# Kernel optimization log

Measured on AMD Instinct MI355X. Metric: run time of the kernel, lower is better.

## Reference

```python
import jax, jax.numpy as jnp
import numpy as np

MARGIN = 0.3
BIG = 9999999.0


def setup_inputs() -> dict:
    key = jax.random.key(0)
    k1, k2, k3 = jax.random.split(key, 3)
    N, D, D2, NUM_IDS = 8192, 1024, 512, 512
    emb = jax.random.normal(k1, (N, D), dtype=jnp.float32)
    clot_feats_s = jax.random.normal(k2, (N, D2), dtype=jnp.float32)
    label = jax.random.randint(k3, (N,), 0, NUM_IDS, dtype=jnp.int64)
    return {"emb": emb, "label": label, "clot_feats_s": clot_feats_s}


def _margin_ranking_loss(x1, x2, y, margin):
    # torch MarginRankingLoss: mean(max(0, -y*(x1-x2)+margin))
    return jnp.mean(jnp.maximum(0.0, -y * (x1 - x2) + margin))


def reference(emb, label, clot_feats_s):
    N = emb.shape[0]
    # euclidean_dist(emb, emb): [N,N]
    sq = jnp.sum(emb * emb, axis=1)
    dist = sq[:, None] + sq[None, :] - 2.0 * (emb @ emb.T)
    dist = jnp.sqrt(jnp.clip(dist, 1e-12, None))
    # cosine similarity of clot_feats_s with itself: [N,N]
    nrm = jnp.sqrt(jnp.sum(clot_feats_s * clot_feats_s, axis=1))
    cos = (clot_feats_s @ clot_feats_s.T) / (nrm[:, None] * nrm[None, :])
    # same-identity mask
    sim = (label[:, None] == label[None, :]).astype(dist.dtype)
    # batch-hard: top-2 positives (largest masked distance), hardest negative (smallest)
    pos_vals, pos_idx = jax.lax.top_k(dist - BIG * (1.0 - sim), 2)
    dist_ap1, dist_ap2 = pos_vals[:, 0], pos_vals[:, 1]
    neg_mat = dist + BIG * sim
    hard_n_idx = jnp.argmin(neg_mat, axis=1)
    dist_an = jnp.min(neg_mat, axis=1)
    rows = jnp.arange(N)
    # per-row gathers into cosine-sim matrix (detached in original)
    alpha1 = jax.lax.stop_gradient(cos[rows, pos_idx[:, 0]])
    alpha2 = jax.lax.stop_gradient(cos[rows, pos_idx[:, 1]])
    # (alphan gathered in original but unused in the loss)
    y11 = jnp.where(alpha1 < alpha2, -1.0, 1.0)
    y11_m = jnp.where(alpha1 == alpha2, 0.0, 1.0)
    loss11 = _margin_ranking_loss(
        dist_ap2 * y11_m,
        dist_ap1 * y11_m + MARGIN * (alpha1 - alpha2 - y11),
        y11, MARGIN)
    dist_ap1_m = dist_ap1 + MARGIN * (alpha1 - 1.0)
    loss13 = _margin_ranking_loss(dist_an, dist_ap1_m, 1.0, MARGIN)
    loss = 0.1 * loss11 + loss13
    prec = jnp.mean((dist_an > dist_ap1_m).astype(jnp.float32))
    return loss, prec
```

## Files before the change

kernel.cpp:

```cpp
#include <hip/hip_runtime.h>
#include <stdint.h>

#define NR 8192
#define DE 1024
#define DC 512
#define BIGF 9999999.0f
#define MARG 0.3f
#define NEGI -3.0e38f
#define POSI 3.0e38f

typedef __attribute__((ext_vector_type(8))) short bf16x8;
typedef __attribute__((ext_vector_type(4))) float f32x4;

typedef __attribute__((address_space(3))) unsigned int lds_u32;
typedef const __attribute__((address_space(1))) unsigned int glb_u32;

static __device__ __forceinline__ void ld_g2l16(const void* g, void* l) {
    __builtin_amdgcn_global_load_lds((glb_u32*)g, (lds_u32*)l, 16, 0, 0);
}

static __device__ __forceinline__ unsigned short f2bf(float x) {
    unsigned u = __float_as_uint(x);
    unsigned r = u + 0x7FFFu + ((u >> 16) & 1u);
    return (unsigned short)(r >> 16);
}

static __device__ __forceinline__ float b2f(short u) {
    return __uint_as_float(((unsigned)(unsigned short)u) << 16);
}

__global__ __launch_bounds__(256) void k_prep_emb(const float* __restrict__ emb,
                                                  const int* __restrict__ label,
                                                  short* __restrict__ embb,
                                                  float* __restrict__ sq,
                                                  int* __restrict__ cnt) {
    int row = blockIdx.x, tid = threadIdx.x;
    float4 v = ((const float4*)(emb + (size_t)row * DE))[tid];
    float s = v.x * v.x + v.y * v.y + v.z * v.z + v.w * v.w;
    ushort4 b;
    b.x = f2bf(v.x); b.y = f2bf(v.y); b.z = f2bf(v.z); b.w = f2bf(v.w);
    *(ushort4*)&embb[(size_t)row * DE + tid * 4] = b;
    for (int m = 1; m < 64; m <<= 1) s += __shfl_xor(s, m);
    __shared__ float red[4];
    if ((tid & 63) == 0) red[tid >> 6] = s;
    __syncthreads();
    if (tid == 0) {
        sq[row] = red[0] + red[1] + red[2] + red[3];
        atomicAdd(&cnt[label[row]], 1);
    }
}

__global__ __launch_bounds__(512) void k_scan(const int* __restrict__ cnt,
                                              int* __restrict__ clsOff) {
    __shared__ int s[512];
    int t = threadIdx.x;
    s[t] = cnt[t];
    __syncthreads();
    for (int d = 1; d < 512; d <<= 1) {
        int v = (t >= d) ? s[t - d] : 0;
        __syncthreads();
        s[t] += v;
        __syncthreads();
    }
    clsOff[t] = s[t] - cnt[t];
}

__global__ __launch_bounds__(256) void k_fill(const int* __restrict__ label,
                                              const int* __restrict__ clsOff,
                                              int* __restrict__ fill,
                                              int* __restrict__ list) {
    int i = blockIdx.x * 256 + threadIdx.x;
    int l = label[i];
    int p = atomicAdd(&fill[l], 1);
    list[clsOff[l] + p] = i;
}

__global__ __launch_bounds__(256, 3) void k_main(const short* __restrict__ embb,
                                                 const float* __restrict__ sq,
                                                 const int* __restrict__ label,
                                                 unsigned* __restrict__ mnA) {
    const int L = (blockIdx.x & 7) * 68 + (blockIdx.x >> 3);
    int bx = (int)((sqrtf((float)(1 + 2 * L)) - 1.0f) * 0.5f);
    while (2 * (bx + 1) * (bx + 1) + 2 * (bx + 1) <= L) ++bx;
    while (2 * bx * bx + 2 * bx > L) --bx;
    const int pnl = L - (2 * bx * bx + 2 * bx);
    const int d = pnl - bx * 4;
    const int jt0 = d > 0 ? d : 0;

    __shared__ __align__(16) short As[128 * 32];
    __shared__ __align__(16) short Bs[128 * 32];

    const int tid = threadIdx.x;
    const int lane = tid & 63;
    const int w = tid >> 6;
    const int q = lane >> 4, l15 = lane & 15;
    const int i0 = pnl * 128;

    const int srow = tid >> 2;
    const int g = (tid & 3) ^ ((tid >> 3) & 3);
    const short* gA = embb + (size_t)(i0 + srow) * DE + g * 8;
    const short* gB = embb + (size_t)(bx * 512 + jt0 * 128 + srow) * DE + g * 8;

    const int pxor = q ^ ((l15 >> 1) & 3);

    float rmn[8], sqi[8];
    int lia[8];
#pragma unroll
    for (int pp = 0; pp < 8; ++pp) {
        rmn[pp] = POSI;
        int rowg = i0 + w * 32 + (pp >> 2) * 16 + q * 4 + (pp & 3);
        sqi[pp] = sq[rowg]; lia[pp] = label[rowg];
    }

    auto stage = [&](int koff, const short* gBb) {
        ld_g2l16(gA + koff, &As[(size_t)tid * 8]);
        ld_g2l16(gA + (size_t)64 * DE + koff, &As[(size_t)(tid + 256) * 8]);
        ld_g2l16(gBb + koff, &Bs[(size_t)tid * 8]);
        ld_g2l16(gBb + (size_t)64 * DE + koff, &Bs[(size_t)(tid + 256) * 8]);
    };

    stage(0, gB);

    for (int jt = jt0; jt < 4; ++jt) {
        const int j0 = bx * 512 + jt * 128;
        f32x4 acc[2][8];
#pragma unroll
        for (int mi = 0; mi < 2; ++mi)
#pragma unroll
            for (int ni = 0; ni < 8; ++ni) acc[mi][ni] = (f32x4){0.f, 0.f, 0.f, 0.f};

        for (int ks = 0; ks < 32; ++ks) {
            __syncthreads();
            bf16x8 af[2], bfr[8];
#pragma unroll
            for (int mi = 0; mi < 2; ++mi)
                af[mi] = *(const bf16x8*)&As[(w * 32 + mi * 16 + l15) * 32 + pxor * 8];
#pragma unroll
            for (int ni = 0; ni < 8; ++ni)
                bfr[ni] = *(const bf16x8*)&Bs[(ni * 16 + l15) * 32 + pxor * 8];
#pragma unroll
            for (int mi = 0; mi < 2; ++mi)
#pragma unroll
                for (int ni = 0; ni < 8; ++ni)
                    acc[mi][ni] = __builtin_amdgcn_mfma_f32_16x16x32_bf16(af[mi], bfr[ni], acc[mi][ni], 0, 0, 0);
            __syncthreads();
            if (ks < 31) {
                stage((ks + 1) * 32, gB);
            } else if (jt < 3) {
                gB += (size_t)128 * DE;
                stage(0, gB);
            }
        }

#pragma unroll
        for (int ni = 0; ni < 8; ++ni) {
            const int cg = j0 + ni * 16 + l15;
            const float sqjv = sq[cg];
            const int lbjv = label[cg];
            float cmn = POSI;
#pragma unroll
            for (int pp = 0; pp < 8; ++pp) {
                float d2 = fmaf(-2.0f, acc[pp >> 2][ni][pp & 3], sqi[pp] + sqjv);
                d2 = fmaxf(d2, 1e-12f);
                float dn = (lia[pp] == lbjv) ? POSI : d2;
                rmn[pp] = fminf(rmn[pp], dn);
                cmn = fminf(cmn, dn);
            }
            cmn = fminf(cmn, __shfl_xor(cmn, 16));
            cmn = fminf(cmn, __shfl_xor(cmn, 32));
            if (q == 0) atomicMin(&mnA[cg], __float_as_uint(cmn));
        }
    }

#pragma unroll
    for (int pp = 0; pp < 8; ++pp) {
        float m0 = rmn[pp];
        for (int s = 1; s <= 8; s <<= 1) m0 = fminf(m0, __shfl_xor(m0, s));
        if (l15 == 0) {
            int rowg = i0 + w * 32 + (pp >> 2) * 16 + q * 4 + (pp & 3);
            atomicMin(&mnA[rowg], __float_as_uint(m0));
        }
    }
}

__global__ __launch_bounds__(256) void k_pos(const short* __restrict__ embb,
                                             const float* __restrict__ sq,
                                             const float* __restrict__ clot,
                                             const int* __restrict__ label,
                                             const int* __restrict__ cnt,
                                             const int* __restrict__ clsOff,
                                             const int* __restrict__ clsList,
                                             const unsigned* __restrict__ mnA,
                                             float* __restrict__ ap1, float* __restrict__ ap2,
                                             float* __restrict__ an,
                                             float* __restrict__ alpha1, float* __restrict__ alpha2) {
    int wid = threadIdx.x >> 6, lane = threadIdx.x & 63;
    int row = blockIdx.x * 4 + wid;
    int lb = label[row];
    int cc = cnt[lb], off = clsOff[lb];
    float sqiv = sq[row];

    const bf16x8* rp = (const bf16x8*)(embb + (size_t)row * DE + lane * 16);
    bf16x8 ra = rp[0], rb = rp[1];
    float rf[16];
#pragma unroll
    for (int t = 0; t < 8; ++t) { rf[t] = b2f(ra[t]); rf[8 + t] = b2f(rb[t]); }

    float v1 = NEGI, v2 = NEGI;
    int i1 = 0, i2 = 0;
    for (int m = 0; m < cc; ++m) {
        int j = clsList[off + m];
        float d2;
        if (j == row) {
            d2 = 1e-12f;
        } else {
            const bf16x8* jp = (const bf16x8*)(embb + (size_t)j * DE + lane * 16);
            bf16x8 ja = jp[0], jb = jp[1];
            float s = 0.f;
#pragma unroll
            for (int t = 0; t < 8; ++t) s = fmaf(rf[t], b2f(ja[t]), s);
#pragma unroll
            for (int t = 0; t < 8; ++t) s = fmaf(rf[8 + t], b2f(jb[t]), s);
            for (int mm = 1; mm < 64; mm <<= 1) s += __shfl_xor(s, mm);
            d2 = fmaxf(fmaf(-2.0f, s, sqiv + sq[j]), 1e-12f);
        }
        bool t1 = (d2 > v1) || (d2 == v1 && j < i1);
        bool t2 = (d2 > v2) || (d2 == v2 && j < i2);
        v2 = t1 ? v1 : (t2 ? d2 : v2);
        i2 = t1 ? i1 : (t2 ? j : i2);
        v1 = t1 ? d2 : v1;
        i1 = t1 ? j : i1;
    }

    float a1 = sqrtf(v1);
    int j1 = i1;
    float a2v; int j2;
    if (cc >= 2) {
        a2v = sqrtf(v2);
        j2 = i2;
    } else {
        float kv = NEGI; int ki = 0;
        for (int c = lane; c < NR; c += 64) {
            if (label[c] == lb) continue;
            float s = 0.f;
            const short* crow = embb + (size_t)c * DE;
            const short* rrow = embb + (size_t)row * DE;
            for (int t = 0; t < DE; ++t) s = fmaf(b2f(rrow[t]), b2f(crow[t]), s);
            float d2c = fmaxf(fmaf(-2.0f, s, sqiv + sq[c]), 1e-12f);
            bool tk = (d2c > kv) || (d2c == kv && c < ki);
            kv = tk ? d2c : kv; ki = tk ? c : ki;
        }
        for (int mm = 1; mm < 64; mm <<= 1) {
            float ov = __shfl_xor(kv, mm); int oi = __shfl_xor(ki, mm);
            bool tk = (ov > kv) || (ov == kv && oi < ki);
            kv = tk ? ov : kv; ki = tk ? oi : ki;
        }
        a2v = sqrtf(kv) - BIGF;
        j2 = ki;
    }

    const float4* c4 = (const float4*)clot;
    float s1 = 0.f, s2 = 0.f, n0 = 0.f, n1 = 0.f, n2 = 0.f;
    for (int t = lane; t < DC / 4; t += 64) {
        float4 a = c4[(size_t)row * (DC / 4) + t];
        float4 b1 = c4[(size_t)j1 * (DC / 4) + t];
        float4 b2 = c4[(size_t)j2 * (DC / 4) + t];
        s1 += a.x * b1.x + a.y * b1.y + a.z * b1.z + a.w * b1.w;
        s2 += a.x * b2.x + a.y * b2.y + a.z * b2.z + a.w * b2.w;
        n0 += a.x * a.x + a.y * a.y + a.z * a.z + a.w * a.w;
        n1 += b1.x * b1.x + b1.y * b1.y + b1.z * b1.z + b1.w * b1.w;
        n2 += b2.x * b2.x + b2.y * b2.y + b2.z * b2.z + b2.w * b2.w;
    }
    for (int mm = 1; mm < 64; mm <<= 1) {
        s1 += __shfl_xor(s1, mm); s2 += __shfl_xor(s2, mm);
        n0 += __shfl_xor(n0, mm); n1 += __shfl_xor(n1, mm); n2 += __shfl_xor(n2, mm);
    }
    if (lane == 0) {
        ap1[row] = a1; ap2[row] = a2v;
        an[row] = sqrtf(__uint_as_float(mnA[row]));
        alpha1[row] = s1 / (sqrtf(n0) * sqrtf(n1));
        alpha2[row] = s2 / (sqrtf(n0) * sqrtf(n2));
    }
}

__global__ __launch_bounds__(256) void k_final(const float* __restrict__ ap1, const float* __restrict__ ap2,
                                               const float* __restrict__ an,
                                               const float* __restrict__ alpha1, const float* __restrict__ alpha2,
                                               float* __restrict__ out) {
    int tid = threadIdx.x;
    float sl11 = 0.f, sl13 = 0.f, sp = 0.f;
    for (int row = tid; row < NR; row += 256) {
        float a1 = alpha1[row], a2 = alpha2[row];
        float dap1 = ap1[row], dap2 = ap2[row], dan = an[row];
        float y = (a1 < a2) ? -1.f : 1.f;
        float ym = (a1 == a2) ? 0.f : 1.f;
        float x1 = dap2 * ym;
        float x2 = dap1 * ym + MARG * (a1 - a2 - y);
        sl11 += fmaxf(0.f, -y * (x1 - x2) + MARG);
        float ap1m = dap1 + MARG * (a1 - 1.f);
        sl13 += fmaxf(0.f, -(dan - ap1m) + MARG);
        sp += (dan > ap1m) ? 1.f : 0.f;
    }
    for (int m = 1; m < 64; m <<= 1) {
        sl11 += __shfl_xor(sl11, m);
        sl13 += __shfl_xor(sl13, m);
        sp += __shfl_xor(sp, m);
    }
    __shared__ float r11[4], r13[4], rp[4];
    if ((tid & 63) == 0) { r11[tid >> 6] = sl11; r13[tid >> 6] = sl13; rp[tid >> 6] = sp; }
    __syncthreads();
    if (tid == 0) {
        float t11 = r11[0] + r11[1] + r11[2] + r11[3];
        float t13 = r13[0] + r13[1] + r13[2] + r13[3];
        float tp = rp[0] + rp[1] + rp[2] + rp[3];
        out[0] = 0.1f * (t11 / (float)NR) + t13 / (float)NR;
        out[1] = tp / (float)NR;
    }
}

extern "C" void kernel_launch(void* const* d_in, const int* in_sizes, int n_in,
                              void* d_out, int out_size, void* d_ws, size_t ws_size,
                              hipStream_t stream) {
    const float* emb = (const float*)d_in[0];
    const int* label = (const int*)d_in[1];
    const float* clot = (const float*)d_in[2];
    float* out = (float*)d_out;

    char* ws = (char*)d_ws;
    size_t off = 0;
    auto alloc = [&](size_t bytes) -> char* {
        char* p = ws + off;
        off = (off + bytes + 255) & ~(size_t)255;
        return p;
    };
    short*    embb = (short*)alloc((size_t)NR * DE * 2);
    float*    sq   = (float*)alloc(NR * 4);
    int*      cnt  = (int*)alloc(512 * 4);
    int*      cOff = (int*)alloc(512 * 4);
    int*      fill = (int*)alloc(512 * 4);
    int*      list = (int*)alloc(NR * 4);
    unsigned* mnA  = (unsigned*)alloc((size_t)NR * 4);
    float*    ap1  = (float*)alloc(NR * 4);
    float*    ap2  = (float*)alloc(NR * 4);
    float*    an   = (float*)alloc(NR * 4);
    float*    al1  = (float*)alloc(NR * 4);
    float*    al2  = (float*)alloc(NR * 4);

    hipMemsetAsync(cnt, 0, 512 * 4, stream);
    hipMemsetAsync(fill, 0, 512 * 4, stream);
    hipMemsetAsync(mnA, 0xFF, (size_t)NR * 4, stream);

    k_prep_emb<<<dim3(NR), dim3(256), 0, stream>>>(emb, label, embb, sq, cnt);
    k_scan<<<dim3(1), dim3(512), 0, stream>>>(cnt, cOff);
    k_fill<<<dim3(NR / 256), dim3(256), 0, stream>>>(label, cOff, fill, list);
    k_main<<<dim3(544), dim3(256), 0, stream>>>(embb, sq, label, mnA);
    k_pos<<<dim3(NR / 4), dim3(256), 0, stream>>>(embb, sq, clot, label, cnt, cOff, list,
                                                  mnA, ap1, ap2, an, al1, al2);
    k_final<<<dim3(1), dim3(256), 0, stream>>>(ap1, ap2, an, al1, al2, out);
}
```

Baseline: 256.9 us.

## Use square 128x128 triangular tiles in main GEMM and per-class positive kernel

The main distance kernel stops having each block sweep a 128x512 strip and gives each block one 128x128 upper-triangular tile. Warps are laid out 2x2 (64x64 each) instead of 4x1, and the launch grows from 544 to 2080 blocks. The positive-mining kernel now runs one block per identity class and stages up to 48 class member embeddings in LDS, so all rows of the class reuse them instead of each row re-reading members from global memory. The trade-off is more blocks with shorter K loops in the GEMM, about 96KB of LDS per block (limiting occupancy), and load imbalance across classes of different size.

New measurement: 381.2 us. 1.48x slower.

```diff
diff --git a/kernel.cpp b/kernel.cpp
--- a/kernel.cpp
+++ b/kernel.cpp
@@ -8,6 +8,7 @@
 #define MARG 0.3f
 #define NEGI -3.0e38f
 #define POSI 3.0e38f
+#define CAPR 48
 
 typedef __attribute__((ext_vector_type(8))) short bf16x8;
 typedef __attribute__((ext_vector_type(4))) float f32x4;
@@ -79,13 +80,14 @@
                                                  const float* __restrict__ sq,
                                                  const int* __restrict__ label,
                                                  unsigned* __restrict__ mnA) {
-    const int L = (blockIdx.x & 7) * 68 + (blockIdx.x >> 3);
-    int bx = (int)((sqrtf((float)(1 + 2 * L)) - 1.0f) * 0.5f);
-    while (2 * (bx + 1) * (bx + 1) + 2 * (bx + 1) <= L) ++bx;
-    while (2 * bx * bx + 2 * bx > L) --bx;
-    const int pnl = L - (2 * bx * bx + 2 * bx);
-    const int d = pnl - bx * 4;
-    const int jt0 = d > 0 ? d : 0;
+    const int b = blockIdx.x;
+    int r = (int)((129.0f - sqrtf(16641.0f - 8.0f * (float)b)) * 0.5f);
+    if (r < 0) r = 0;
+    if (r > 63) r = 63;
+    while (r > 0 && 64 * r - (r * (r - 1)) / 2 > b) --r;
+    while (64 * (r + 1) - ((r + 1) * r) / 2 <= b) ++r;
+    const int c = r + (b - (64 * r - (r * (r - 1)) / 2));
+    const int i0 = r * 128, j0 = c * 128;
 
     __shared__ __align__(16) short As[128 * 32];
     __shared__ __align__(16) short Bs[128 * 32];
@@ -93,93 +95,91 @@
     const int tid = threadIdx.x;
     const int lane = tid & 63;
     const int w = tid >> 6;
+    const int wr = w >> 1, wc = w & 1;
     const int q = lane >> 4, l15 = lane & 15;
-    const int i0 = pnl * 128;
 
     const int srow = tid >> 2;
     const int g = (tid & 3) ^ ((tid >> 3) & 3);
     const short* gA = embb + (size_t)(i0 + srow) * DE + g * 8;
-    const short* gB = embb + (size_t)(bx * 512 + jt0 * 128 + srow) * DE + g * 8;
+    const short* gB = embb + (size_t)(j0 + srow) * DE + g * 8;
 
     const int pxor = q ^ ((l15 >> 1) & 3);
 
-    float rmn[8], sqi[8];
-    int lia[8];
-#pragma unroll
-    for (int pp = 0; pp < 8; ++pp) {
-        rmn[pp] = POSI;
-        int rowg = i0 + w * 32 + (pp >> 2) * 16 + q * 4 + (pp & 3);
-        sqi[pp] = sq[rowg]; lia[pp] = label[rowg];
-    }
-
-    auto stage = [&](int koff, const short* gBb) {
+    auto stage = [&](int koff) {
         ld_g2l16(gA + koff, &As[(size_t)tid * 8]);
         ld_g2l16(gA + (size_t)64 * DE + koff, &As[(size_t)(tid + 256) * 8]);
-        ld_g2l16(gBb + koff, &Bs[(size_t)tid * 8]);
-        ld_g2l16(gBb + (size_t)64 * DE + koff, &Bs[(size_t)(tid + 256) * 8]);
+        ld_g2l16(gB + koff, &Bs[(size_t)tid * 8]);
+        ld_g2l16(gB + (size_t)64 * DE + koff, &Bs[(size_t)(tid + 256) * 8]);
     };
 
-    stage(0, gB);
-
-    for (int jt = jt0; jt < 4; ++jt) {
-        const int j0 = bx * 512 + jt * 128;
-        f32x4 acc[2][8];
-#pragma unroll
-        for (int mi = 0; mi < 2; ++mi)
-#pragma unroll
-            for (int ni = 0; ni < 8; ++ni) acc[mi][ni] = (f32x4){0.f, 0.f, 0.f, 0.f};
-
-        for (int ks = 0; ks < 32; ++ks) {
-            __syncthreads();
-            bf16x8 af[2], bfr[8];
-#pragma unroll
-            for (int mi = 0; mi < 2; ++mi)
-                af[mi] = *(const bf16x8*)&As[(w * 32 + mi * 16 + l15) * 32 + pxor * 8];
-#pragma unroll
-            for (int ni = 0; ni < 8; ++ni)
-                bfr[ni] = *(const bf16x8*)&Bs[(ni * 16 + l15) * 32 + pxor * 8];
-#pragma unroll
-            for (int mi = 0; mi < 2; ++mi)
-#pragma unroll
-                for (int ni = 0; ni < 8; ++ni)
-                    acc[mi][ni] = __builtin_amdgcn_mfma_f32_16x16x32_bf16(af[mi], bfr[ni], acc[mi][ni], 0, 0, 0);
-            __syncthreads();
-            if (ks < 31) {
-                stage((ks + 1) * 32, gB);
-            } else if (jt < 3) {
-                gB += (size_t)128 * DE;
-                stage(0, gB);
+    stage(0);
+
+    f32x4 acc[4][4];
+#pragma unroll
+    for (int mi = 0; mi < 4; ++mi)
+#pragma unroll
+        for (int ni = 0; ni < 4; ++ni) acc[mi][ni] = (f32x4){0.f, 0.f, 0.f, 0.f};
+
+    for (int ks = 0; ks < 32; ++ks) {
+        __syncthreads();
+        bf16x8 af[4], bfr[4];
+#pragma unroll
+        for (int mi = 0; mi < 4; ++mi)
+            af[mi] = *(const bf16x8*)&As[(wr * 64 + mi * 16 + l15) * 32 + pxor * 8];
+#pragma unroll
+        for (int ni = 0; ni < 4; ++ni)
+            bfr[ni] = *(const bf16x8*)&Bs[(wc * 64 + ni * 16 + l15) * 32 + pxor * 8];
+#pragma unroll
+        for (int mi = 0; mi < 4; ++mi)
+#pragma unroll
+            for (int ni = 0; ni < 4; ++ni)
+                acc[mi][ni] = __builtin_amdgcn_mfma_f32_16x16x32_bf16(af[mi], bfr[ni], acc[mi][ni], 0, 0, 0);
+        __syncthreads();
+        if (ks < 31) stage((ks + 1) * 32);
+    }
+
+    const int rb = i0 + wr * 64, cb = j0 + wc * 64;
+    float sqj[4]; int lbj[4]; float cmn[4];
+#pragma unroll
+    for (int ni = 0; ni < 4; ++ni) {
+        int cg = cb + ni * 16 + l15;
+        sqj[ni] = sq[cg]; lbj[ni] = label[cg]; cmn[ni] = POSI;
+    }
+#pragma unroll
+    for (int mi = 0; mi < 4; ++mi) {
+        float rm[4] = {POSI, POSI, POSI, POSI};
+        float sqi[4]; int lbi[4];
+#pragma unroll
+        for (int rr = 0; rr < 4; ++rr) {
+            int rg = rb + mi * 16 + q * 4 + rr;
+            sqi[rr] = sq[rg]; lbi[rr] = label[rg];
+        }
+#pragma unroll
+        for (int ni = 0; ni < 4; ++ni)
+#pragma unroll
+            for (int rr = 0; rr < 4; ++rr) {
+                float d2 = fmaf(-2.0f, acc[mi][ni][rr], sqi[rr] + sqj[ni]);
+                d2 = fmaxf(d2, 1e-12f);
+                float dn = (lbi[rr] == lbj[ni]) ? POSI : d2;
+                rm[rr] = fminf(rm[rr], dn);
+                cmn[ni] = fminf(cmn[ni], dn);
             }
-        }
-
-#pragma unroll
-        for (int ni = 0; ni < 8; ++ni) {
-            const int cg = j0 + ni * 16 + l15;
-            const float sqjv = sq[cg];
-            const int lbjv = label[cg];
-            float cmn = POSI;
-#pragma unroll
-            for (int pp = 0; pp < 8; ++pp) {
-                float d2 = fmaf(-2.0f, acc[pp >> 2][ni][pp & 3], sqi[pp] + sqjv);
-                d2 = fmaxf(d2, 1e-12f);
-                float dn = (lia[pp] == lbjv) ? POSI : d2;
-                rmn[pp] = fminf(rmn[pp], dn);
-                cmn = fminf(cmn, dn);
-            }
-            cmn = fminf(cmn, __shfl_xor(cmn, 16));
-            cmn = fminf(cmn, __shfl_xor(cmn, 32));
-            if (q == 0) atomicMin(&mnA[cg], __float_as_uint(cmn));
-        }
-    }
-
-#pragma unroll
-    for (int pp = 0; pp < 8; ++pp) {
-        float m0 = rmn[pp];
-        for (int s = 1; s <= 8; s <<= 1) m0 = fminf(m0, __shfl_xor(m0, s));
-        if (l15 == 0) {
-            int rowg = i0 + w * 32 + (pp >> 2) * 16 + q * 4 + (pp & 3);
-            atomicMin(&mnA[rowg], __float_as_uint(m0));
-        }
+#pragma unroll
+        for (int rr = 0; rr < 4; ++rr) {
+            float v = rm[rr];
+            v = fminf(v, __shfl_xor(v, 1));
+            v = fminf(v, __shfl_xor(v, 2));
+            v = fminf(v, __shfl_xor(v, 4));
+            v = fminf(v, __shfl_xor(v, 8));
+            if (l15 == 0) atomicMin(&mnA[rb + mi * 16 + q * 4 + rr], __float_as_uint(v));
+        }
+    }
+#pragma unroll
+    for (int ni = 0; ni < 4; ++ni) {
+        float v = cmn[ni];
+        v = fminf(v, __shfl_xor(v, 16));
+        v = fminf(v, __shfl_xor(v, 32));
+        if (q == 0) atomicMin(&mnA[cb + ni * 16 + l15], __float_as_uint(v));
     }
 }
 
@@ -194,92 +194,116 @@
                                              float* __restrict__ ap1, float* __restrict__ ap2,
                                              float* __restrict__ an,
                                              float* __restrict__ alpha1, float* __restrict__ alpha2) {
-    int wid = threadIdx.x >> 6, lane = threadIdx.x & 63;
-    int row = blockIdx.x * 4 + wid;
-    int lb = label[row];
-    int cc = cnt[lb], off = clsOff[lb];
-    float sqiv = sq[row];
-
-    const bf16x8* rp = (const bf16x8*)(embb + (size_t)row * DE + lane * 16);
-    bf16x8 ra = rp[0], rb = rp[1];
-    float rf[16];
-#pragma unroll
-    for (int t = 0; t < 8; ++t) { rf[t] = b2f(ra[t]); rf[8 + t] = b2f(rb[t]); }
-
-    float v1 = NEGI, v2 = NEGI;
-    int i1 = 0, i2 = 0;
-    for (int m = 0; m < cc; ++m) {
-        int j = clsList[off + m];
-        float d2;
-        if (j == row) {
-            d2 = 1e-12f;
+    const int cls = blockIdx.x;
+    const int cc = cnt[cls], off = clsOff[cls];
+    if (cc == 0) return;
+
+    __shared__ __align__(16) short Ls[CAPR * DE];
+    __shared__ int gidS[256];
+    __shared__ float sqS[256];
+
+    const int tid = threadIdx.x, wid = tid >> 6, lane = tid & 63;
+    const int ccap = cc < 256 ? cc : 256;
+    for (int m = tid; m < ccap; m += 256) {
+        int gid = clsList[off + m];
+        gidS[m] = gid;
+        sqS[m] = sq[gid];
+    }
+    __syncthreads();
+    const int nst = cc < CAPR ? cc : CAPR;
+    for (int idx = tid; idx < nst * 128; idx += 256) {
+        int m = idx >> 7, ch = idx & 127;
+        *(int4*)&Ls[m * DE + ch * 8] = *(const int4*)&embb[(size_t)gidS[m] * DE + ch * 8];
+    }
+    __syncthreads();
+
+    for (int m = wid; m < cc; m += 4) {
+        const int gm = (m < 256) ? gidS[m] : clsList[off + m];
+        const float sqm = (m < 256) ? sqS[m] : sq[gm];
+        const short* mrow = (m < CAPR) ? (const short*)&Ls[m * DE] : &embb[(size_t)gm * DE];
+        bf16x8 ra = *(const bf16x8*)&mrow[lane * 16];
+        bf16x8 rbv = *(const bf16x8*)&mrow[lane * 16 + 8];
+        float rf[16];
+#pragma unroll
+        for (int t = 0; t < 8; ++t) { rf[t] = b2f(ra[t]); rf[8 + t] = b2f(rbv[t]); }
+
+        float v1 = NEGI, v2 = NEGI;
+        int i1 = 0, i2 = 0;
+        for (int jm = 0; jm < cc; ++jm) {
+            const int gj = (jm < 256) ? gidS[jm] : clsList[off + jm];
+            float d2;
+            if (jm == m) {
+                d2 = 1e-12f;
+            } else {
+                const short* jrow = (jm < CAPR) ? (const short*)&Ls[jm * DE] : &embb[(size_t)gj * DE];
+                bf16x8 ja = *(const bf16x8*)&jrow[lane * 16];
+                bf16x8 jb = *(const bf16x8*)&jrow[lane * 16 + 8];
+                float s = 0.f;
+#pragma unroll
+                for (int t = 0; t < 8; ++t) s = fmaf(rf[t], b2f(ja[t]), s);
+#pragma unroll
+                for (int t = 0; t < 8; ++t) s = fmaf(rf[8 + t], b2f(jb[t]), s);
+                for (int mm = 1; mm < 64; mm <<= 1) s += __shfl_xor(s, mm);
+                const float sqj = (jm < 256) ? sqS[jm] : sq[gj];
+                d2 = fmaxf(fmaf(-2.0f, s, sqm + sqj), 1e-12f);
+            }
+            bool t1 = (d2 > v1) || (d2 == v1 && gj < i1);
+            bool t2 = (d2 > v2) || (d2 == v2 && gj < i2);
+            v2 = t1 ? v1 : (t2 ? d2 : v2);
+            i2 = t1 ? i1 : (t2 ? gj : i2);
+            v1 = t1 ? d2 : v1;
+            i1 = t1 ? gj : i1;
+        }
+
+        float a1 = sqrtf(v1);
+        int j1 = i1;
+        float a2v; int j2;
+        if (cc >= 2) {
+            a2v = sqrtf(v2);
+            j2 = i2;
         } else {
-            const bf16x8* jp = (const bf16x8*)(embb + (size_t)j * DE + lane * 16);
-            bf16x8 ja = jp[0], jb = jp[1];
-            float s = 0.f;
-#pragma unroll
-            for (int t = 0; t < 8; ++t) s = fmaf(rf[t], b2f(ja[t]), s);
-#pragma unroll
-            for (int t = 0; t < 8; ++t) s = fmaf(rf[8 + t], b2f(jb[t]), s);
-            for (int mm = 1; mm < 64; mm <<= 1) s += __shfl_xor(s, mm);
-            d2 = fmaxf(fmaf(-2.0f, s, sqiv + sq[j]), 1e-12f);
-        }
-        bool t1 = (d2 > v1) || (d2 == v1 && j < i1);
-        bool t2 = (d2 > v2) || (d2 == v2 && j < i2);
-        v2 = t1 ? v1 : (t2 ? d2 : v2);
-        i2 = t1 ? i1 : (t2 ? j : i2);
-        v1 = t1 ? d2 : v1;
-        i1 = t1 ? j : i1;
-    }
-
-    float a1 = sqrtf(v1);
-    int j1 = i1;
-    float a2v; int j2;
-    if (cc >= 2) {
-        a2v = sqrtf(v2);
-        j2 = i2;
-    } else {
-        float kv = NEGI; int ki = 0;
-        for (int c = lane; c < NR; c += 64) {
-            if (label[c] == lb) continue;
-            float s = 0.f;
-            const short* crow = embb + (size_t)c * DE;
-            const short* rrow = embb + (size_t)row * DE;
-            for (int t = 0; t < DE; ++t) s = fmaf(b2f(rrow[t]), b2f(crow[t]), s);
-            float d2c = fmaxf(fmaf(-2.0f, s, sqiv + sq[c]), 1e-12f);
-            bool tk = (d2c > kv) || (d2c == kv && c < ki);
-            kv = tk ? d2c : kv; ki = tk ? c : ki;
+            float kv = NEGI; int ki = 0;
+            for (int cr = lane; cr < NR; cr += 64) {
+                if (label[cr] == cls) continue;
+                float s = 0.f;
+                const short* crow = embb + (size_t)cr * DE;
+                const short* rrow = embb + (size_t)gm * DE;
+                for (int t = 0; t < DE; ++t) s = fmaf(b2f(rrow[t]), b2f(crow[t]), s);
+                float d2c = fmaxf(fmaf(-2.0f, s, sqm + sq[cr]), 1e-12f);
+                bool tk = (d2c > kv) || (d2c == kv && cr < ki);
+                kv = tk ? d2c : kv; ki = tk ? cr : ki;
+            }
+            for (int mm = 1; mm < 64; mm <<= 1) {
+                float ov = __shfl_xor(kv, mm); int oi = __shfl_xor(ki, mm);
+                bool tk = (ov > kv) || (ov == kv && oi < ki);
+                kv = tk ? ov : kv; ki = tk ? oi : ki;
+            }
+            a2v = sqrtf(kv) - BIGF;
+            j2 = ki;
+        }
+
+        const float4* c4 = (const float4*)clot;
+        float s1 = 0.f, s2 = 0.f, n0 = 0.f, n1 = 0.f, n2 = 0.f;
+        for (int t = lane; t < DC / 4; t += 64) {
+            float4 a = c4[(size_t)gm * (DC / 4) + t];
+            float4 b1 = c4[(size_t)j1 * (DC / 4) + t];
+            float4 b2 = c4[(size_t)j2 * (DC / 4) + t];
+            s1 += a.x * b1.x + a.y * b1.y + a.z * b1.z + a.w * b1.w;
+            s2 += a.x * b2.x + a.y * b2.y + a.z * b2.z + a.w * b2.w;
+            n0 += a.x * a.x + a.y * a.y + a.z * a.z + a.w * a.w;
+            n1 += b1.x * b1.x + b1.y * b1.y + b1.z * b1.z + b1.w * b1.w;
+            n2 += b2.x * b2.x + b2.y * b2.y + b2.z * b2.z + b2.w * b2.w;
         }
         for (int mm = 1; mm < 64; mm <<= 1) {
-            float ov = __shfl_xor(kv, mm); int oi = __shfl_xor(ki, mm);
-            bool tk = (ov > kv) || (ov == kv && oi < ki);
-            kv = tk ? ov : kv; ki = tk ? oi : ki;
-        }
-        a2v = sqrtf(kv) - BIGF;
-        j2 = ki;
-    }
-
-    const float4* c4 = (const float4*)clot;
-    float s1 = 0.f, s2 = 0.f, n0 = 0.f, n1 = 0.f, n2 = 0.f;
-    for (int t = lane; t < DC / 4; t += 64) {
-        float4 a = c4[(size_t)row * (DC / 4) + t];
-        float4 b1 = c4[(size_t)j1 * (DC / 4) + t];
-        float4 b2 = c4[(size_t)j2 * (DC / 4) + t];
-        s1 += a.x * b1.x + a.y * b1.y + a.z * b1.z + a.w * b1.w;
-        s2 += a.x * b2.x + a.y * b2.y + a.z * b2.z + a.w * b2.w;
-        n0 += a.x * a.x + a.y * a.y + a.z * a.z + a.w * a.w;
-        n1 += b1.x * b1.x + b1.y * b1.y + b1.z * b1.z + b1.w * b1.w;
-        n2 += b2.x * b2.x + b2.y * b2.y + b2.z * b2.z + b2.w * b2.w;
-    }
-    for (int mm = 1; mm < 64; mm <<= 1) {
-        s1 += __shfl_xor(s1, mm); s2 += __shfl_xor(s2, mm);
-        n0 += __shfl_xor(n0, mm); n1 += __shfl_xor(n1, mm); n2 += __shfl_xor(n2, mm);
-    }
-    if (lane == 0) {
-        ap1[row] = a1; ap2[row] = a2v;
-        an[row] = sqrtf(__uint_as_float(mnA[row]));
-        alpha1[row] = s1 / (sqrtf(n0) * sqrtf(n1));
-        alpha2[row] = s2 / (sqrtf(n0) * sqrtf(n2));
+            s1 += __shfl_xor(s1, mm); s2 += __shfl_xor(s2, mm);
+            n0 += __shfl_xor(n0, mm); n1 += __shfl_xor(n1, mm); n2 += __shfl_xor(n2, mm);
+        }
+        if (lane == 0) {
+            ap1[gm] = a1; ap2[gm] = a2v;
+            an[gm] = sqrtf(__uint_as_float(mnA[gm]));
+            alpha1[gm] = s1 / (sqrtf(n0) * sqrtf(n1));
+            alpha2[gm] = s2 / (sqrtf(n0) * sqrtf(n2));
+        }
     }
 }
 
@@ -353,8 +377,8 @@
     k_prep_emb<<<dim3(NR), dim3(256), 0, stream>>>(emb, label, embb, sq, cnt);
     k_scan<<<dim3(1), dim3(512), 0, stream>>>(cnt, cOff);
     k_fill<<<dim3(NR / 256), dim3(256), 0, stream>>>(label, cOff, fill, list);
-    k_main<<<dim3(544), dim3(256), 0, stream>>>(embb, sq, label, mnA);
-    k_pos<<<dim3(NR / 4), dim3(256), 0, stream>>>(embb, sq, clot, label, cnt, cOff, list,
-                                                  mnA, ap1, ap2, an, al1, al2);
+    k_main<<<dim3(2080), dim3(256), 0, stream>>>(embb, sq, label, mnA);
+    k_pos<<<dim3(512), dim3(256), 0, stream>>>(embb, sq, clot, label, cnt, cOff, list,
+                                               mnA, ap1, ap2, an, al1, al2);
     k_final<<<dim3(1), dim3(256), 0, stream>>>(ap1, ap2, an, al1, al2, out);
 }
```
